# Kernel optimization log

Hardware: AMD Instinct MI355X
Metric: run time of the kernel (lower is better)

Reference implementation:

```python
import jax, jax.numpy as jnp
import numpy as np

N_NODES = 100000
N_EDGES = 1000000
D_FEAT = 64


def setup_inputs() -> dict:
    key = jax.random.key(0)
    k1, k2, k3 = jax.random.split(key, 3)
    embeddings = jax.random.normal(k1, (N_NODES, D_FEAT), dtype=jnp.float32)
    src = jax.random.randint(k2, (N_EDGES,), 0, N_NODES, dtype=jnp.int32)
    dst = jax.random.randint(k3, (N_EDGES,), 0, N_NODES, dtype=jnp.int32)
    return {"embeddings": embeddings, "src": src, "dst": dst}


def reference(embeddings, src, dst):
    # DGL update_all(copy_src('h','m'), mean('m','h')):
    # gather source features per edge, then mean-aggregate by destination.
    msgs = embeddings[src]                                    # [E, D]
    summed = jax.ops.segment_sum(msgs, dst, num_segments=N_NODES)   # [N, D]
    counts = jax.ops.segment_sum(jnp.ones((src.shape[0],), jnp.float32), dst,
                                 num_segments=N_NODES)        # [N]
    # nodes with no in-edges get 0 (DGL mean-of-empty semantics)
    denom = jnp.maximum(counts, 1.0)[:, None]
    return summed / denom
```

## Files before the change

kernel.cpp:

```cpp
#include <hip/hip_runtime.h>
#include <hip/hip_fp16.h>

#define N_NODES 100000
#define N_EDGES 1000000
#define D_FEAT  64

#define BIN_SHIFT 6
#define BIN_NODES 64
#define NBINS ((N_NODES + BIN_NODES - 1) >> BIN_SHIFT)
#define BIN_CAP 1152

#define NCHUNK 128
#define CHUNK_E ((N_EDGES + NCHUNK - 1) / NCHUNK)
#define CELL 24
#define CCAP_E 23

#define WS_BUCKET_INTS ((size_t)NCHUNK * NBINS * CELL)
#define WS_EMB16       WS_BUCKET_INTS
#define WS_NEEDED      ((WS_BUCKET_INTS + (size_t)N_NODES * D_FEAT / 2) * sizeof(int))

__global__ __launch_bounds__(1024) void prep_kernel(const float* __restrict__ emb,
                                                    const int* __restrict__ src,
                                                    const int* __restrict__ dst,
                                                    int* __restrict__ ws) {
    int tid = threadIdx.x;
    if (blockIdx.x < NCHUNK) {
        __shared__ int h[NBINS];
        for (int j = tid; j < NBINS; j += 1024) h[j] = 0;
        __syncthreads();
        int c  = blockIdx.x;
        int e0 = c * CHUNK_E, e1 = min(N_EDGES, e0 + CHUNK_E);
        int* __restrict__ cells = ws + (size_t)c * NBINS * CELL;
        for (int e = e0 + tid; e < e1; e += 1024) {
            int d = dst[e], s = src[e];
            int bin = d >> BIN_SHIFT;
            int slot = atomicAdd(&h[bin], 1);
            if (slot < CCAP_E)
                cells[bin * CELL + 1 + slot] = ((d & (BIN_NODES - 1)) << 17) | s;
        }
        __syncthreads();
        for (int j = tid; j < NBINS; j += 1024)
            cells[j * CELL] = min(h[j], CCAP_E);
    } else {
        __half2* __restrict__ e16 = (__half2*)(ws + WS_EMB16);
        const float4* __restrict__ e32 = (const float4*)emb;
        const int total4 = N_NODES * D_FEAT / 4;
        int start = (blockIdx.x - NCHUNK) * 1024 + tid;
        for (int i = start; i < total4; i += NCHUNK * 1024) {
            float4 v = e32[i];
            e16[2 * i]     = __floats2half2_rn(v.x, v.y);
            e16[2 * i + 1] = __floats2half2_rn(v.z, v.w);
        }
    }
}

__global__ __launch_bounds__(512) void fused_gather_kernel(const int* __restrict__ ws,
                                                           float* __restrict__ out) {
    __shared__ int s_edges[BIN_CAP];
    __shared__ int s_sorted[BIN_CAP];
    __shared__ int s_rcnt[NCHUNK];
    __shared__ int s_roff[NCHUNK];
    __shared__ int s_hist[BIN_NODES];
    __shared__ int s_off[BIN_NODES];
    __shared__ int s_cur[BIN_NODES];
    __shared__ int s_alloc;

    const char* __restrict__ emb16 = (const char*)(ws + WS_EMB16);
    int b   = blockIdx.x;
    int tid = threadIdx.x;

    if (tid < BIN_NODES) s_hist[tid] = 0;
    if (tid == 0) s_alloc = 0;
    __syncthreads();

    if (tid < NCHUNK) {
        int cnt = ws[((size_t)tid * NBINS + b) * CELL];
        s_rcnt[tid] = cnt;
        s_roff[tid] = atomicAdd(&s_alloc, cnt);
    }
    __syncthreads();
    int total = s_alloc;
    if (total > BIN_CAP) total = BIN_CAP;

    {
        int g = tid >> 2, li = tid & 3;
        int cg = s_rcnt[g], og = s_roff[g];
        const int* __restrict__ cell = ws + ((size_t)g * NBINS + b) * CELL + 1;
        for (int i = li; i < cg; i += 4) {
            int o = og + i;
            if (o < BIN_CAP) {
                int p = cell[i];
                s_edges[o] = p;
                atomicAdd(&s_hist[p >> 17], 1);
            }
        }
    }
    __syncthreads();

    if (tid < 64) {
        int v = s_hist[tid];
        int incl = v;
        #pragma unroll
        for (int o = 1; o < 64; o <<= 1) {
            int t = __shfl_up(incl, o);
            if (tid >= o) incl += t;
        }
        s_off[tid] = incl - v;
        s_cur[tid] = incl - v;
    }
    __syncthreads();

    for (int i = tid; i < total; i += 512) {
        int p = s_edges[i];
        s_sorted[atomicAdd(&s_cur[p >> 17], 1)] = p & 0x1FFFF;
    }
    __syncthreads();

    int wave = tid >> 6, lane = tid & 63;
    int sub  = lane >> 4;
    int fq   = lane & 15;
    const int fb = fq << 3;

    #pragma unroll
    for (int pr = 0; pr < 4; ++pr) {
        int lnA = wave * 8 + pr * 2;
        int lnB = lnA + 1;
        int degA = s_hist[lnA], offA = s_off[lnA];
        int degB = s_hist[lnB], offB = s_off[lnB];

        float4 accA = make_float4(0.f, 0.f, 0.f, 0.f);
        float4 accB = make_float4(0.f, 0.f, 0.f, 0.f);

        int iA = sub, iB = sub;
        for (; iA + 12 < degA; iA += 16) {
            uint2 u0 = *(const uint2*)(emb16 + ((size_t)s_sorted[offA + iA]      << 7) + fb);
            uint2 u1 = *(const uint2*)(emb16 + ((size_t)s_sorted[offA + iA + 4]  << 7) + fb);
            uint2 u2 = *(const uint2*)(emb16 + ((size_t)s_sorted[offA + iA + 8]  << 7) + fb);
            uint2 u3 = *(const uint2*)(emb16 + ((size_t)s_sorted[offA + iA + 12] << 7) + fb);
            float2 f;
            f = __half22float2(*(__half2*)&u0.x); accA.x += f.x; accA.y += f.y;
            f = __half22float2(*(__half2*)&u0.y); accA.z += f.x; accA.w += f.y;
            f = __half22float2(*(__half2*)&u1.x); accA.x += f.x; accA.y += f.y;
            f = __half22float2(*(__half2*)&u1.y); accA.z += f.x; accA.w += f.y;
            f = __half22float2(*(__half2*)&u2.x); accA.x += f.x; accA.y += f.y;
            f = __half22float2(*(__half2*)&u2.y); accA.z += f.x; accA.w += f.y;
            f = __half22float2(*(__half2*)&u3.x); accA.x += f.x; accA.y += f.y;
            f = __half22float2(*(__half2*)&u3.y); accA.z += f.x; accA.w += f.y;
        }
        for (; iB + 12 < degB; iB += 16) {
            uint2 u0 = *(const uint2*)(emb16 + ((size_t)s_sorted[offB + iB]      << 7) + fb);
            uint2 u1 = *(const uint2*)(emb16 + ((size_t)s_sorted[offB + iB + 4]  << 7) + fb);
            uint2 u2 = *(const uint2*)(emb16 + ((size_t)s_sorted[offB + iB + 8]  << 7) + fb);
            uint2 u3 = *(const uint2*)(emb16 + ((size_t)s_sorted[offB + iB + 12] << 7) + fb);
            float2 f;
            f = __half22float2(*(__half2*)&u0.x); accB.x += f.x; accB.y += f.y;
            f = __half22float2(*(__half2*)&u0.y); accB.z += f.x; accB.w += f.y;
            f = __half22float2(*(__half2*)&u1.x); accB.x += f.x; accB.y += f.y;
            f = __half22float2(*(__half2*)&u1.y); accB.z += f.x; accB.w += f.y;
            f = __half22float2(*(__half2*)&u2.x); accB.x += f.x; accB.y += f.y;
            f = __half22float2(*(__half2*)&u2.y); accB.z += f.x; accB.w += f.y;
            f = __half22float2(*(__half2*)&u3.x); accB.x += f.x; accB.y += f.y;
            f = __half22float2(*(__half2*)&u3.y); accB.z += f.x; accB.w += f.y;
        }
        {
            uint2 a0 = make_uint2(0u, 0u), a1 = a0, a2 = a0;
            uint2 b0 = a0, b1 = a0, b2 = a0;
            if (iA < degA)     a0 = *(const uint2*)(emb16 + ((size_t)s_sorted[offA + iA]     << 7) + fb);
            if (iA + 4 < degA) a1 = *(const uint2*)(emb16 + ((size_t)s_sorted[offA + iA + 4] << 7) + fb);
            if (iA + 8 < degA) a2 = *(const uint2*)(emb16 + ((size_t)s_sorted[offA + iA + 8] << 7) + fb);
            if (iB < degB)     b0 = *(const uint2*)(emb16 + ((size_t)s_sorted[offB + iB]     << 7) + fb);
            if (iB + 4 < degB) b1 = *(const uint2*)(emb16 + ((size_t)s_sorted[offB + iB + 4] << 7) + fb);
            if (iB + 8 < degB) b2 = *(const uint2*)(emb16 + ((size_t)s_sorted[offB + iB + 8] << 7) + fb);
            float2 f;
            f = __half22float2(*(__half2*)&a0.x); accA.x += f.x; accA.y += f.y;
            f = __half22float2(*(__half2*)&a0.y); accA.z += f.x; accA.w += f.y;
            f = __half22float2(*(__half2*)&a1.x); accA.x += f.x; accA.y += f.y;
            f = __half22float2(*(__half2*)&a1.y); accA.z += f.x; accA.w += f.y;
            f = __half22float2(*(__half2*)&a2.x); accA.x += f.x; accA.y += f.y;
            f = __half22float2(*(__half2*)&a2.y); accA.z += f.x; accA.w += f.y;
            f = __half22float2(*(__half2*)&b0.x); accB.x += f.x; accB.y += f.y;
            f = __half22float2(*(__half2*)&b0.y); accB.z += f.x; accB.w += f.y;
            f = __half22float2(*(__half2*)&b1.x); accB.x += f.x; accB.y += f.y;
            f = __half22float2(*(__half2*)&b1.y); accB.z += f.x; accB.w += f.y;
            f = __half22float2(*(__half2*)&b2.x); accB.x += f.x; accB.y += f.y;
            f = __half22float2(*(__half2*)&b2.y); accB.z += f.x; accB.w += f.y;
        }

        #pragma unroll
        for (int m = 16; m < 64; m <<= 1) {
            accA.x += __shfl_xor(accA.x, m);  accB.x += __shfl_xor(accB.x, m);
            accA.y += __shfl_xor(accA.y, m);  accB.y += __shfl_xor(accB.y, m);
            accA.z += __shfl_xor(accA.z, m);  accB.z += __shfl_xor(accB.z, m);
            accA.w += __shfl_xor(accA.w, m);  accB.w += __shfl_xor(accB.w, m);
        }

        if (sub == 0) {
            int nodeA = (b << BIN_SHIFT) + lnA;
            int nodeB = (b << BIN_SHIFT) + lnB;
            float invA = 1.0f / (float)max(degA, 1);
            float invB = 1.0f / (float)max(degB, 1);
            accA.x *= invA; accA.y *= invA; accA.z *= invA; accA.w *= invA;
            accB.x *= invB; accB.y *= invB; accB.z *= invB; accB.w *= invB;
            if (nodeA < N_NODES)
                *(float4*)(out + (size_t)nodeA * D_FEAT + fq * 4) = accA;
            if (nodeB < N_NODES)
                *(float4*)(out + (size_t)nodeB * D_FEAT + fq * 4) = accB;
        }
    }
}


__global__ void gcn_zero_kernel(float* __restrict__ out, float* __restrict__ counts) {
    int stride = gridDim.x * blockDim.x;
    int i = blockIdx.x * blockDim.x + threadIdx.x;
    const int total = N_NODES * D_FEAT;
    for (int idx = i; idx < total; idx += stride) out[idx] = 0.0f;
    for (int idx = i; idx < N_NODES; idx += stride) counts[idx] = 0.0f;
}

__global__ void gcn_scatter_kernel(const float* __restrict__ emb,
                                   const int* __restrict__ src,
                                   const int* __restrict__ dst,
                                   float* __restrict__ out,
                                   float* __restrict__ counts) {
    int gid  = blockIdx.x * blockDim.x + threadIdx.x;
    int edge = gid >> 6;
    int lane = gid & 63;
    if (edge >= N_EDGES) return;
    int s = src[edge];
    int d = dst[edge];
    float v = emb[(size_t)s * D_FEAT + lane];
    atomicAdd(&out[(size_t)d * D_FEAT + lane], v);
    if (lane == 0) atomicAdd(&counts[d], 1.0f);
}

__global__ void gcn_norm_kernel(float* __restrict__ out,
                                const float* __restrict__ counts) {
    int i = blockIdx.x * blockDim.x + threadIdx.x;
    if (i >= N_NODES * D_FEAT) return;
    int n = i >> 6;
    float c = counts[n];
    out[i] *= (1.0f / fmaxf(c, 1.0f));
}


extern "C" void kernel_launch(void* const* d_in, const int* in_sizes, int n_in,
                              void* d_out, int out_size, void* d_ws, size_t ws_size,
                              hipStream_t stream) {
    const float* emb = (const float*)d_in[0];
    const int*   src = (const int*)d_in[1];
    const int*   dst = (const int*)d_in[2];
    float* out = (float*)d_out;

    if (ws_size >= WS_NEEDED) {
        int* ws = (int*)d_ws;
        prep_kernel<<<2 * NCHUNK, 1024, 0, stream>>>(emb, src, dst, ws);
        fused_gather_kernel<<<NBINS, 512, 0, stream>>>(ws, out);
    } else {
        float* counts = (float*)d_ws;
        gcn_zero_kernel<<<2048, 256, 0, stream>>>(out, counts);
        const int scatter_blocks = (N_EDGES * 64) / 256;
        gcn_scatter_kernel<<<scatter_blocks, 256, 0, stream>>>(emb, src, dst, out, counts);
        const int norm_blocks = (N_NODES * D_FEAT + 255) / 256;
        gcn_norm_kernel<<<norm_blocks, 256, 0, stream>>>(out, counts);
    }
}
```

Measured before the change: 54.06 us.

## Use 16-byte half-precision gathers with 8 lanes per row and more chunks

The gather phase changes from 16 lanes reading 8 bytes each to 8 lanes reading 16 bytes each. That gives 8 edge slots per wave, and each wave now handles one destination node at a time instead of interleaving two. Edge bucketing doubles the number of chunks and shrinks the cells, so the prep stage has more parallelism and the per-bin merge step reads smaller cells. In exchange, memory-level parallelism across paired nodes is lost, the shuffle-reduction tree gets deeper, and the bucket workspace grows.

```diff
diff --git a/kernel.cpp b/kernel.cpp
--- a/kernel.cpp
+++ b/kernel.cpp
@@ -10,10 +10,10 @@
 #define NBINS ((N_NODES + BIN_NODES - 1) >> BIN_SHIFT)
 #define BIN_CAP 1152
 
-#define NCHUNK 128
+#define NCHUNK 256
 #define CHUNK_E ((N_EDGES + NCHUNK - 1) / NCHUNK)
-#define CELL 24
-#define CCAP_E 23
+#define CELL 16
+#define CCAP_E 15
 
 #define WS_BUCKET_INTS ((size_t)NCHUNK * NBINS * CELL)
 #define WS_EMB16       WS_BUCKET_INTS
@@ -83,10 +83,10 @@
     if (total > BIN_CAP) total = BIN_CAP;
 
     {
-        int g = tid >> 2, li = tid & 3;
+        int g = tid >> 1, li = tid & 1;
         int cg = s_rcnt[g], og = s_roff[g];
         const int* __restrict__ cell = ws + ((size_t)g * NBINS + b) * CELL + 1;
-        for (int i = li; i < cg; i += 4) {
+        for (int i = li; i < cg; i += 2) {
             int o = og + i;
             if (o < BIN_CAP) {
                 int p = cell[i];
@@ -117,94 +117,64 @@
     __syncthreads();
 
     int wave = tid >> 6, lane = tid & 63;
-    int sub  = lane >> 4;
-    int fq   = lane & 15;
-    const int fb = fq << 3;
+    int sub  = lane >> 3;
+    int f8   = lane & 7;
+    const int fb = f8 << 4;
 
     #pragma unroll
-    for (int pr = 0; pr < 4; ++pr) {
-        int lnA = wave * 8 + pr * 2;
-        int lnB = lnA + 1;
-        int degA = s_hist[lnA], offA = s_off[lnA];
-        int degB = s_hist[lnB], offB = s_off[lnB];
-
-        float4 accA = make_float4(0.f, 0.f, 0.f, 0.f);
-        float4 accB = make_float4(0.f, 0.f, 0.f, 0.f);
-
-        int iA = sub, iB = sub;
-        for (; iA + 12 < degA; iA += 16) {
-            uint2 u0 = *(const uint2*)(emb16 + ((size_t)s_sorted[offA + iA]      << 7) + fb);
-            uint2 u1 = *(const uint2*)(emb16 + ((size_t)s_sorted[offA + iA + 4]  << 7) + fb);
-            uint2 u2 = *(const uint2*)(emb16 + ((size_t)s_sorted[offA + iA + 8]  << 7) + fb);
-            uint2 u3 = *(const uint2*)(emb16 + ((size_t)s_sorted[offA + iA + 12] << 7) + fb);
+    for (int ln0 = 0; ln0 < 8; ++ln0) {
+        int ln  = wave * 8 + ln0;
+        int deg = s_hist[ln];
+        int off = s_off[ln];
+
+        float4 accLo = make_float4(0.f, 0.f, 0.f, 0.f);
+        float4 accHi = make_float4(0.f, 0.f, 0.f, 0.f);
+
+        int i = sub;
+        for (; i + 8 < deg; i += 16) {
+            uint4 u0 = *(const uint4*)(emb16 + ((size_t)s_sorted[off + i]     << 7) + fb);
+            uint4 u1 = *(const uint4*)(emb16 + ((size_t)s_sorted[off + i + 8] << 7) + fb);
             float2 f;
-            f = __half22float2(*(__half2*)&u0.x); accA.x += f.x; accA.y += f.y;
-            f = __half22float2(*(__half2*)&u0.y); accA.z += f.x; accA.w += f.y;
-            f = __half22float2(*(__half2*)&u1.x); accA.x += f.x; accA.y += f.y;
-            f = __half22float2(*(__half2*)&u1.y); accA.z += f.x; accA.w += f.y;
-            f = __half22float2(*(__half2*)&u2.x); accA.x += f.x; accA.y += f.y;
-            f = __half22float2(*(__half2*)&u2.y); accA.z += f.x; accA.w += f.y;
-            f = __half22float2(*(__half2*)&u3.x); accA.x += f.x; accA.y += f.y;
-            f = __half22float2(*(__half2*)&u3.y); accA.z += f.x; accA.w += f.y;
-        }
-        for (; iB + 12 < degB; iB += 16) {
-            uint2 u0 = *(const uint2*)(emb16 + ((size_t)s_sorted[offB + iB]      << 7) + fb);
-            uint2 u1 = *(const uint2*)(emb16 + ((size_t)s_sorted[offB + iB + 4]  << 7) + fb);
-            uint2 u2 = *(const uint2*)(emb16 + ((size_t)s_sorted[offB + iB + 8]  << 7) + fb);
-            uint2 u3 = *(const uint2*)(emb16 + ((size_t)s_sorted[offB + iB + 12] << 7) + fb);
+            f = __half22float2(*(__half2*)&u0.x); accLo.x += f.x; accLo.y += f.y;
+            f = __half22float2(*(__half2*)&u0.y); accLo.z += f.x; accLo.w += f.y;
+            f = __half22float2(*(__half2*)&u0.z); accHi.x += f.x; accHi.y += f.y;
+            f = __half22float2(*(__half2*)&u0.w); accHi.z += f.x; accHi.w += f.y;
+            f = __half22float2(*(__half2*)&u1.x); accLo.x += f.x; accLo.y += f.y;
+            f = __half22float2(*(__half2*)&u1.y); accLo.z += f.x; accLo.w += f.y;
+            f = __half22float2(*(__half2*)&u1.z); accHi.x += f.x; accHi.y += f.y;
+            f = __half22float2(*(__half2*)&u1.w); accHi.z += f.x; accHi.w += f.y;
+        }
+        if (i < deg) {
+            uint4 u0 = *(const uint4*)(emb16 + ((size_t)s_sorted[off + i] << 7) + fb);
             float2 f;
-            f = __half22float2(*(__half2*)&u0.x); accB.x += f.x; accB.y += f.y;
-            f = __half22float2(*(__half2*)&u0.y); accB.z += f.x; accB.w += f.y;
-            f = __half22float2(*(__half2*)&u1.x); accB.x += f.x; accB.y += f.y;
-            f = __half22float2(*(__half2*)&u1.y); accB.z += f.x; accB.w += f.y;
-            f = __half22float2(*(__half2*)&u2.x); accB.x += f.x; accB.y += f.y;
-            f = __half22float2(*(__half2*)&u2.y); accB.z += f.x; accB.w += f.y;
-            f = __half22float2(*(__half2*)&u3.x); accB.x += f.x; accB.y += f.y;
-            f = __half22float2(*(__half2*)&u3.y); accB.z += f.x; accB.w += f.y;
-        }
-        {
-            uint2 a0 = make_uint2(0u, 0u), a1 = a0, a2 = a0;
-            uint2 b0 = a0, b1 = a0, b2 = a0;
-            if (iA < degA)     a0 = *(const uint2*)(emb16 + ((size_t)s_sorted[offA + iA]     << 7) + fb);
-            if (iA + 4 < degA) a1 = *(const uint2*)(emb16 + ((size_t)s_sorted[offA + iA + 4] << 7) + fb);
-            if (iA + 8 < degA) a2 = *(const uint2*)(emb16 + ((size_t)s_sorted[offA + iA + 8] << 7) + fb);
-            if (iB < degB)     b0 = *(const uint2*)(emb16 + ((size_t)s_sorted[offB + iB]     << 7) + fb);
-            if (iB + 4 < degB) b1 = *(const uint2*)(emb16 + ((size_t)s_sorted[offB + iB + 4] << 7) + fb);
-            if (iB + 8 < degB) b2 = *(const uint2*)(emb16 + ((size_t)s_sorted[offB + iB + 8] << 7) + fb);
-            float2 f;
-            f = __half22float2(*(__half2*)&a0.x); accA.x += f.x; accA.y += f.y;
-            f = __half22float2(*(__half2*)&a0.y); accA.z += f.x; accA.w += f.y;
-            f = __half22float2(*(__half2*)&a1.x); accA.x += f.x; accA.y += f.y;
-            f = __half22float2(*(__half2*)&a1.y); accA.z += f.x; accA.w += f.y;
-            f = __half22float2(*(__half2*)&a2.x); accA.x += f.x; accA.y += f.y;
-            f = __half22float2(*(__half2*)&a2.y); accA.z += f.x; accA.w += f.y;
-            f = __half22float2(*(__half2*)&b0.x); accB.x += f.x; accB.y += f.y;
-            f = __half22float2(*(__half2*)&b0.y); accB.z += f.x; accB.w += f.y;
-            f = __half22float2(*(__half2*)&b1.x); accB.x += f.x; accB.y += f.y;
-            f = __half22float2(*(__half2*)&b1.y); accB.z += f.x; accB.w += f.y;
-            f = __half22float2(*(__half2*)&b2.x); accB.x += f.x; accB.y += f.y;
-            f = __half22float2(*(__half2*)&b2.y); accB.z += f.x; accB.w += f.y;
+            f = __half22float2(*(__half2*)&u0.x); accLo.x += f.x; accLo.y += f.y;
+            f = __half22float2(*(__half2*)&u0.y); accLo.z += f.x; accLo.w += f.y;
+            f = __half22float2(*(__half2*)&u0.z); accHi.x += f.x; accHi.y += f.y;
+            f = __half22float2(*(__half2*)&u0.w); accHi.z += f.x; accHi.w += f.y;
         }
 
         #pragma unroll
-        for (int m = 16; m < 64; m <<= 1) {
-            accA.x += __shfl_xor(accA.x, m);  accB.x += __shfl_xor(accB.x, m);
-            accA.y += __shfl_xor(accA.y, m);  accB.y += __shfl_xor(accB.y, m);
-            accA.z += __shfl_xor(accA.z, m);  accB.z += __shfl_xor(accB.z, m);
-            accA.w += __shfl_xor(accA.w, m);  accB.w += __shfl_xor(accB.w, m);
+        for (int m = 8; m < 64; m <<= 1) {
+            accLo.x += __shfl_xor(accLo.x, m);
+            accLo.y += __shfl_xor(accLo.y, m);
+            accLo.z += __shfl_xor(accLo.z, m);
+            accLo.w += __shfl_xor(accLo.w, m);
+            accHi.x += __shfl_xor(accHi.x, m);
+            accHi.y += __shfl_xor(accHi.y, m);
+            accHi.z += __shfl_xor(accHi.z, m);
+            accHi.w += __shfl_xor(accHi.w, m);
         }
 
         if (sub == 0) {
-            int nodeA = (b << BIN_SHIFT) + lnA;
-            int nodeB = (b << BIN_SHIFT) + lnB;
-            float invA = 1.0f / (float)max(degA, 1);
-            float invB = 1.0f / (float)max(degB, 1);
-            accA.x *= invA; accA.y *= invA; accA.z *= invA; accA.w *= invA;
-            accB.x *= invB; accB.y *= invB; accB.z *= invB; accB.w *= invB;
-            if (nodeA < N_NODES)
-                *(float4*)(out + (size_t)nodeA * D_FEAT + fq * 4) = accA;
-            if (nodeB < N_NODES)
-                *(float4*)(out + (size_t)nodeB * D_FEAT + fq * 4) = accB;
+            int node = (b << BIN_SHIFT) + ln;
+            if (node < N_NODES) {
+                float inv = 1.0f / (float)max(deg, 1);
+                accLo.x *= inv; accLo.y *= inv; accLo.z *= inv; accLo.w *= inv;
+                accHi.x *= inv; accHi.y *= inv; accHi.z *= inv; accHi.w *= inv;
+                float* orow = out + (size_t)node * D_FEAT + f8 * 8;
+                *(float4*)(orow)     = accLo;
+                *(float4*)(orow + 4) = accHi;
+            }
         }
     }
 }
```

New measurement: 72.66 us. 34.4% more time.

## Replace fixed-capacity bucket cells with per-chunk counting-sorted edge runs

Applied to the files above, without the earlier changes.

The prep kernel now stages each chunk's edges in shared memory, builds a per-bin histogram, and scans it to offsets. It then writes the edges contiguously sorted by bin, with 16-bit count and prefix tables laid out bin-major. The gather kernel reads those tables coalesced and fetches each chunk's run for its bin. This removes the sparse, padded 24-int cell layout and the edge-dropping capacity limit, shrinking workspace traffic. In exchange prep gains a second pass, a serial 64-lane scan and extra syncs.

```diff
diff --git a/kernel.cpp b/kernel.cpp
--- a/kernel.cpp
+++ b/kernel.cpp
@@ -12,12 +12,13 @@
 
 #define NCHUNK 128
 #define CHUNK_E ((N_EDGES + NCHUNK - 1) / NCHUNK)
-#define CELL 24
-#define CCAP_E 23
-
-#define WS_BUCKET_INTS ((size_t)NCHUNK * NBINS * CELL)
-#define WS_EMB16       WS_BUCKET_INTS
-#define WS_NEEDED      ((WS_BUCKET_INTS + (size_t)N_NODES * D_FEAT / 2) * sizeof(int))
+#define PCHUNK 7936
+
+#define WS_CNT    0
+#define WS_PF     (NBINS * NCHUNK / 2)
+#define WS_BUCKET (NBINS * NCHUNK)
+#define WS_EMB16  (WS_BUCKET + NCHUNK * PCHUNK)
+#define WS_NEEDED ((size_t)(WS_EMB16 + (size_t)N_NODES * D_FEAT / 2) * sizeof(int))
 
 __global__ __launch_bounds__(1024) void prep_kernel(const float* __restrict__ emb,
                                                     const int* __restrict__ src,
@@ -26,21 +27,50 @@
     int tid = threadIdx.x;
     if (blockIdx.x < NCHUNK) {
         __shared__ int h[NBINS];
+        __shared__ unsigned short s_bin[CHUNK_E];
+        __shared__ int s_pack[CHUNK_E];
         for (int j = tid; j < NBINS; j += 1024) h[j] = 0;
         __syncthreads();
         int c  = blockIdx.x;
-        int e0 = c * CHUNK_E, e1 = min(N_EDGES, e0 + CHUNK_E);
-        int* __restrict__ cells = ws + (size_t)c * NBINS * CELL;
-        for (int e = e0 + tid; e < e1; e += 1024) {
-            int d = dst[e], s = src[e];
+        int e0 = c * CHUNK_E;
+        int n  = min(N_EDGES, e0 + CHUNK_E) - e0;
+        for (int i = tid; i < n; i += 1024) {
+            int d = dst[e0 + i], s = src[e0 + i];
             int bin = d >> BIN_SHIFT;
-            int slot = atomicAdd(&h[bin], 1);
-            if (slot < CCAP_E)
-                cells[bin * CELL + 1 + slot] = ((d & (BIN_NODES - 1)) << 17) | s;
-        }
-        __syncthreads();
+            s_bin[i]  = (unsigned short)bin;
+            s_pack[i] = ((d & (BIN_NODES - 1)) << 17) | s;
+            atomicAdd(&h[bin], 1);
+        }
+        __syncthreads();
+        unsigned short* CNT = (unsigned short*)(ws + WS_CNT);
         for (int j = tid; j < NBINS; j += 1024)
-            cells[j * CELL] = min(h[j], CCAP_E);
+            CNT[j * NCHUNK + c] = (unsigned short)h[j];
+        __syncthreads();
+        if (tid < 64) {
+            int lane = tid, carry = 0;
+            for (int cb = 0; cb < NBINS; cb += 64) {
+                int idx = cb + lane;
+                int v = (idx < NBINS) ? h[idx] : 0;
+                int incl = v;
+                #pragma unroll
+                for (int o = 1; o < 64; o <<= 1) {
+                    int t = __shfl_up(incl, o);
+                    if (lane >= o) incl += t;
+                }
+                if (idx < NBINS) h[idx] = carry + incl - v;
+                carry += __shfl(incl, 63);
+            }
+        }
+        __syncthreads();
+        unsigned short* PF = (unsigned short*)(ws + WS_PF);
+        for (int j = tid; j < NBINS; j += 1024)
+            PF[j * NCHUNK + c] = (unsigned short)h[j];
+        __syncthreads();
+        int* __restrict__ run = ws + WS_BUCKET + c * PCHUNK;
+        for (int i = tid; i < n; i += 1024) {
+            int slot = atomicAdd(&h[s_bin[i]], 1);
+            run[slot] = s_pack[i];
+        }
     } else {
         __half2* __restrict__ e16 = (__half2*)(ws + WS_EMB16);
         const float4* __restrict__ e32 = (const float4*)emb;
@@ -60,6 +90,7 @@
     __shared__ int s_sorted[BIN_CAP];
     __shared__ int s_rcnt[NCHUNK];
     __shared__ int s_roff[NCHUNK];
+    __shared__ int s_rbase[NCHUNK];
     __shared__ int s_hist[BIN_NODES];
     __shared__ int s_off[BIN_NODES];
     __shared__ int s_cur[BIN_NODES];
@@ -74,9 +105,13 @@
     __syncthreads();
 
     if (tid < NCHUNK) {
-        int cnt = ws[((size_t)tid * NBINS + b) * CELL];
-        s_rcnt[tid] = cnt;
-        s_roff[tid] = atomicAdd(&s_alloc, cnt);
+        const unsigned short* CNT = (const unsigned short*)(ws + WS_CNT);
+        const unsigned short* PF  = (const unsigned short*)(ws + WS_PF);
+        int cnt = (int)CNT[b * NCHUNK + tid];
+        int pf  = (int)PF[b * NCHUNK + tid];
+        s_rcnt[tid]  = cnt;
+        s_rbase[tid] = tid * PCHUNK + pf;
+        s_roff[tid]  = atomicAdd(&s_alloc, cnt);
     }
     __syncthreads();
     int total = s_alloc;
@@ -85,11 +120,11 @@
     {
         int g = tid >> 2, li = tid & 3;
         int cg = s_rcnt[g], og = s_roff[g];
-        const int* __restrict__ cell = ws + ((size_t)g * NBINS + b) * CELL + 1;
+        const int* __restrict__ run = ws + WS_BUCKET + s_rbase[g];
         for (int i = li; i < cg; i += 4) {
             int o = og + i;
             if (o < BIN_CAP) {
-                int p = cell[i];
+                int p = run[i];
                 s_edges[o] = p;
                 atomicAdd(&s_hist[p >> 17], 1);
             }
```

Result: slower. 56.17 us (+3.9%).
